# Kernel optimization log

Hardware: AMD Instinct MI355X
Metric: run time of the kernel (lower is better)

## Reference

```python
import jax, jax.numpy as jnp
import numpy as np

TABLE_SIZE = 2 ** 18  # log2_hashmap_size = 18
N_LEVELS = 8
PRIME_Y = np.uint32(2654435761)
PRIME_Z = np.uint32(805459861)
# 8 cube-corner offsets in {0,1}^3
CORNERS = jnp.asarray([[(c >> d) & 1 for d in range(3)] for c in range(8)], dtype=jnp.int32)  # [8,3]


def setup_inputs() -> dict:
    key = jax.random.key(0)
    ks = jax.random.split(key, 6)
    N = 2_097_152
    x = jax.random.uniform(ks[0], (N, 3), dtype=jnp.float32)          # points in [0,1]^3
    mesh_min = jnp.zeros((3,), jnp.float32)
    mesh_max = jnp.ones((3,), jnp.float32)
    # tcnn initializes grid features uniform in [-1e-4, 1e-4]
    tables = jax.random.uniform(ks[1], (N_LEVELS, TABLE_SIZE, 2), jnp.float32, -1e-4, 1e-4)
    w_in = jax.random.normal(ks[2], (16, 64), jnp.float32) * (1.0 / np.sqrt(16))
    w_hidden = jax.random.normal(ks[3], (3, 64, 64), jnp.float32) * (1.0 / np.sqrt(64))
    w_out = jax.random.normal(ks[4], (64, 1), jnp.float32) * (1.0 / np.sqrt(64))
    return {"x": x, "mesh_min": mesh_min, "mesh_max": mesh_max,
            "tables": tables, "w_in": w_in, "w_hidden": w_hidden, "w_out": w_out}


def _hashgrid_encode(u, tables):
    """u: [N,3] in [0,1]. tables: [L, T, F]. Returns [N, L*F]."""
    feats = []
    for l in range(N_LEVELS):
        res = 2 * (2 ** l)  # base_resolution=2, per_level_scale=2
        pos = u * res                                   # [N,3]
        c0 = jnp.floor(pos).astype(jnp.int32)
        w = pos - c0                                    # trilinear fractions, [N,3]
        corners = jnp.clip(c0[:, None, :] + CORNERS[None], 0, res)  # [N,8,3]
        if (res + 1) ** 3 <= TABLE_SIZE:
            # dense grid: no hashing needed at coarse levels
            idx = (corners[..., 0]
                   + corners[..., 1] * (res + 1)
                   + corners[..., 2] * (res + 1) ** 2)
        else:
            uc = corners.astype(jnp.uint32)
            h = uc[..., 0] ^ (uc[..., 1] * PRIME_Y) ^ (uc[..., 2] * PRIME_Z)
            idx = (h % jnp.uint32(TABLE_SIZE)).astype(jnp.int32)
        # trilinear weights per corner: prod over dims of w or (1-w)
        wt = jnp.prod(jnp.where(CORNERS[None] == 1, w[:, None, :], 1.0 - w[:, None, :]), axis=-1)  # [N,8]
        feats.append(jnp.einsum('nc,ncf->nf', wt, tables[l][idx]))  # [N,F]
    return jnp.concatenate(feats, axis=-1)  # [N, L*F] = [N,16]


def reference(x, mesh_min, mesh_max, tables, w_in, w_hidden, w_out):
    u = (x - mesh_min) / (mesh_max - mesh_min)          # normalize to [0,1]^3
    enc = _hashgrid_encode(u, tables)                   # [N,16]
    h = jax.nn.relu(enc @ w_in)                         # [N,64]
    for i in range(w_hidden.shape[0]):                  # 3 more hidden layers (4 total)
        h = jax.nn.relu(h @ w_hidden[i])
    out = (h @ w_out).squeeze(-1)                       # [N], no output activation
    return out
```

## Files before the change

kernel.cpp:

```cpp
#include <hip/hip_runtime.h>
#include <stdint.h>

typedef _Float16 half2v __attribute__((ext_vector_type(2)));
typedef _Float16 half4 __attribute__((ext_vector_type(4)));
typedef _Float16 half8 __attribute__((ext_vector_type(8)));
typedef float floatx4 __attribute__((ext_vector_type(4)));
typedef float float4u __attribute__((ext_vector_type(4), aligned(8)));

#define TPB 256
#define ENC_ROW 20

__device__ __forceinline__ half2v pkrtz(float a, float b) {
    return __builtin_bit_cast(half2v, __builtin_amdgcn_cvt_pkrtz(a, b));
}

__device__ __forceinline__ half4 relu_pack(floatx4 c) {
    half2v lo = pkrtz(fmaxf(c[0], 0.f), fmaxf(c[1], 0.f));
    half2v hi = pkrtz(fmaxf(c[2], 0.f), fmaxf(c[3], 0.f));
    half4 r;
    r[0] = lo[0]; r[1] = lo[1]; r[2] = hi[0]; r[3] = hi[1];
    return r;
}

__global__ void prep_weights(const float* __restrict__ w_in,
                             const float* __restrict__ w_hidden,
                             _Float16* __restrict__ ws) {
    int i = blockIdx.x * 256 + threadIdx.x;
    if (i < 1024) {
        int j = i & 3, lane = (i >> 2) & 63, mt = i >> 8;
        int k = ((lane >> 4) & 3) * 4 + j;
        int n = mt * 16 + (lane & 15);
        ws[i] = (_Float16)w_in[k * 64 + n];
    } else if (i < 13312) {
        int t = i - 1024;
        int j = t & 3, lane = (t >> 2) & 63;
        int mt = (t >> 8) & 3, kt = (t >> 10) & 3, layer = t >> 12;
        int k = kt * 16 + ((lane >> 4) & 3) * 4 + j;
        int n = mt * 16 + (lane & 15);
        ws[i] = (_Float16)w_hidden[layer * 4096 + k * 64 + n];
    }
}

__global__ void prep_tables(const float* __restrict__ tables,
                            uint32_t* __restrict__ tf) {
    int i = blockIdx.x * 256 + threadIdx.x;
    float2 v = ((const float2*)tables)[i];
    half2v h;
    h[0] = (_Float16)(v.x * 8192.f);
    h[1] = (_Float16)(v.y * 8192.f);
    tf[i] = __builtin_bit_cast(uint32_t, h);
}

__global__ __launch_bounds__(TPB, 4) void fused_kernel(
    const float* __restrict__ x,
    const float* __restrict__ mesh_min,
    const float* __restrict__ mesh_max,
    const float* __restrict__ tables,
    const uint32_t* __restrict__ tabs,
    const _Float16* __restrict__ ws,
    const float* __restrict__ w_out,
    float* __restrict__ out,
    int N) {
    __shared__ float2 ltab[881];
    __shared__ uint32_t l3tab[4913];
    __shared__ _Float16 encbuf[4][64][ENC_ROW];

    const int wave = threadIdx.x >> 6;
    const int lane = threadIdx.x & 63;
    const int l15 = lane & 15;
    const int quad = lane >> 4;
    const int wavebase = blockIdx.x * TPB + wave * 64;
    const int p = wavebase + lane;

    {
        const float2* t0 = (const float2*)tables;
        for (int i = threadIdx.x; i < 27; i += TPB) ltab[i] = t0[i];
        const float2* t1 = (const float2*)(tables + 1 * 524288);
        for (int i = threadIdx.x; i < 125; i += TPB) ltab[27 + i] = t1[i];
        const float2* t2 = (const float2*)(tables + 2 * 524288);
        for (int i = threadIdx.x; i < 729; i += TPB) ltab[152 + i] = t2[i];
        const uint32_t* t3 = tabs + 3 * 262144;
        for (int i = threadIdx.x; i < 4913; i += TPB) l3tab[i] = t3[i];
    }

    float mn0 = mesh_min[0], mn1 = mesh_min[1], mn2 = mesh_min[2];
    float mx0 = mesh_max[0], mx1 = mesh_max[1], mx2 = mesh_max[2];
    float ux = (x[3 * p + 0] - mn0) / (mx0 - mn0);
    float uy = (x[3 * p + 1] - mn1) / (mx1 - mn1);
    float uz = (x[3 * p + 2] - mn2) / (mx2 - mn2);

    float ef[16];
    float wl[3][3];
    uint32_t g[24];
    uint32_t g4[8];
    float w4x, w4y, w4z;

#pragma unroll
    for (int l = 0; l < 3; ++l) {
        const int res = 64 << l;
        const uint32_t* tab = tabs + (size_t)(l + 5) * 262144;
        float px = ux * (float)res, py = uy * (float)res, pz = uz * (float)res;
        int cx = (int)floorf(px), cy = (int)floorf(py), cz = (int)floorf(pz);
        wl[l][0] = px - (float)cx;
        wl[l][1] = py - (float)cy;
        wl[l][2] = pz - (float)cz;
        uint32_t hy0 = (uint32_t)cy * 2654435761u, hy1 = (uint32_t)(cy + 1) * 2654435761u;
        uint32_t hz0 = (uint32_t)cz * 805459861u,  hz1 = (uint32_t)(cz + 1) * 805459861u;
#pragma unroll
        for (int c = 0; c < 4; ++c) {
            uint32_t hyz = ((c & 1) ? hy1 : hy0) ^ ((c & 2) ? hz1 : hz0);
            uint32_t i0 = ((uint32_t)cx ^ hyz) & 262143u;
            uint32_t i1 = ((uint32_t)(cx + 1) ^ hyz) & 262143u;
            g[l * 8 + 2 * c + 0] = tab[i0];
            g[l * 8 + 2 * c + 1] = tab[i1];
        }
    }

    {
        const int res = 32, s = 33;
        const uint32_t* tab = tabs + (size_t)4 * 262144;
        float px = ux * 32.f, py = uy * 32.f, pz = uz * 32.f;
        int cx = (int)floorf(px), cy = (int)floorf(py), cz = (int)floorf(pz);
        w4x = px - (float)cx; w4y = py - (float)cy; w4z = pz - (float)cz;
        (void)res;
#pragma unroll
        for (int c = 0; c < 4; ++c) {
            int Y = cy + ((c & 1) ? 1 : 0);
            int Z = cz + ((c & 2) ? 1 : 0);
            int i0 = cx + Y * s + Z * s * s;
            g4[2 * c + 0] = tab[i0];
            g4[2 * c + 1] = tab[i0 + 1];
        }
    }

    __syncthreads();

#pragma unroll
    for (int l = 0; l < 3; ++l) {
        const int res = 2 << l;
        const int s = res + 1;
        const int base = (l == 0) ? 0 : (l == 1) ? 27 : 152;
        float px = ux * (float)res, py = uy * (float)res, pz = uz * (float)res;
        int cx = (int)floorf(px), cy = (int)floorf(py), cz = (int)floorf(pz);
        float wx = px - (float)cx, wy = py - (float)cy, wz = pz - (float)cz;
        float f0 = 0.f, f1 = 0.f;
#pragma unroll
        for (int c = 0; c < 4; ++c) {
            int i0 = base + cx + (cy + ((c & 1) ? 1 : 0)) * s + (cz + ((c & 2) ? 1 : 0)) * s * s;
            float wyz = ((c & 1) ? wy : 1.f - wy) * ((c & 2) ? wz : 1.f - wz);
            float2 e0 = ltab[i0];
            float2 e1 = ltab[i0 + 1];
            f0 += wyz * (e0.x + wx * (e1.x - e0.x));
            f1 += wyz * (e0.y + wx * (e1.y - e0.y));
        }
        ef[2 * l + 0] = f0 * 8192.f;
        ef[2 * l + 1] = f1 * 8192.f;
    }

    {
        const int s = 17;
        float px = ux * 16.f, py = uy * 16.f, pz = uz * 16.f;
        int cx = (int)floorf(px), cy = (int)floorf(py), cz = (int)floorf(pz);
        float wx = px - (float)cx, wy = py - (float)cy, wz = pz - (float)cz;
        float f0 = 0.f, f1 = 0.f;
#pragma unroll
        for (int c = 0; c < 4; ++c) {
            int i0 = cx + (cy + ((c & 1) ? 1 : 0)) * s + (cz + ((c & 2) ? 1 : 0)) * s * s;
            float wyz = ((c & 1) ? wy : 1.f - wy) * ((c & 2) ? wz : 1.f - wz);
            half2v e0 = __builtin_bit_cast(half2v, l3tab[i0]);
            half2v e1 = __builtin_bit_cast(half2v, l3tab[i0 + 1]);
            f0 += wyz * ((float)e0[0] + wx * ((float)e1[0] - (float)e0[0]));
            f1 += wyz * ((float)e0[1] + wx * ((float)e1[1] - (float)e0[1]));
        }
        ef[6] = f0;
        ef[7] = f1;
    }

    {
        float f0 = 0.f, f1 = 0.f;
#pragma unroll
        for (int c = 0; c < 4; ++c) {
            float wyz = ((c & 1) ? w4y : 1.f - w4y) * ((c & 2) ? w4z : 1.f - w4z);
            half2v e0 = __builtin_bit_cast(half2v, g4[2 * c + 0]);
            half2v e1 = __builtin_bit_cast(half2v, g4[2 * c + 1]);
            f0 += wyz * ((float)e0[0] + w4x * ((float)e1[0] - (float)e0[0]));
            f1 += wyz * ((float)e0[1] + w4x * ((float)e1[1] - (float)e0[1]));
        }
        ef[8] = f0;
        ef[9] = f1;
    }

#pragma unroll
    for (int l = 0; l < 3; ++l) {
        float wx = wl[l][0], wy = wl[l][1], wz = wl[l][2];
        float f0 = 0.f, f1 = 0.f;
#pragma unroll
        for (int c = 0; c < 4; ++c) {
            float wyz = ((c & 1) ? wy : 1.f - wy) * ((c & 2) ? wz : 1.f - wz);
            half2v e0 = __builtin_bit_cast(half2v, g[l * 8 + 2 * c + 0]);
            half2v e1 = __builtin_bit_cast(half2v, g[l * 8 + 2 * c + 1]);
            f0 += wyz * ((float)e0[0] + wx * ((float)e1[0] - (float)e0[0]));
            f1 += wyz * ((float)e0[1] + wx * ((float)e1[1] - (float)e0[1]));
        }
        ef[10 + 2 * l + 0] = f0;
        ef[10 + 2 * l + 1] = f1;
    }

#pragma unroll
    for (int v = 0; v < 4; ++v) {
        half2v lo = pkrtz(ef[4 * v + 0], ef[4 * v + 1]);
        half2v hi = pkrtz(ef[4 * v + 2], ef[4 * v + 3]);
        half4 t;
        t[0] = lo[0]; t[1] = lo[1]; t[2] = hi[0]; t[3] = hi[1];
        *(half4*)&encbuf[wave][lane][v * 4] = t;
    }

    floatx4 C[4][4];
    {
        half4 b[4];
#pragma unroll
        for (int nt = 0; nt < 4; ++nt)
            b[nt] = *(const half4*)&encbuf[wave][nt * 16 + l15][quad * 4];
#pragma unroll
        for (int mt = 0; mt < 4; ++mt) {
            half4 a = *(const half4*)(ws + mt * 256 + lane * 4);
#pragma unroll
            for (int nt = 0; nt < 4; ++nt) {
                floatx4 zero = {0.f, 0.f, 0.f, 0.f};
                C[mt][nt] = __builtin_amdgcn_mfma_f32_16x16x16f16(a, b[nt], zero, 0, 0, 0);
            }
        }
    }

#pragma unroll
    for (int layer = 0; layer < 3; ++layer) {
        half4 b[4][4];
#pragma unroll
        for (int kt = 0; kt < 4; ++kt)
#pragma unroll
            for (int nt = 0; nt < 4; ++nt)
                b[kt][nt] = relu_pack(C[kt][nt]);
#pragma unroll
        for (int mt = 0; mt < 4; ++mt) {
            half4 a[4];
#pragma unroll
            for (int kt = 0; kt < 4; ++kt)
                a[kt] = *(const half4*)(ws + 1024 + ((layer * 4 + kt) * 4 + mt) * 256 + lane * 4);
#pragma unroll
            for (int nt = 0; nt < 4; ++nt) {
                floatx4 acc = {0.f, 0.f, 0.f, 0.f};
#pragma unroll
                for (int kt = 0; kt < 4; ++kt)
                    acc = __builtin_amdgcn_mfma_f32_16x16x16f16(a[kt], b[kt][nt], acc, 0, 0, 0);
                C[mt][nt] = acc;
            }
        }
    }

    {
        float s[4] = {0.f, 0.f, 0.f, 0.f};
#pragma unroll
        for (int mt = 0; mt < 4; ++mt) {
            float4 wo = *(const float4*)(w_out + mt * 16 + quad * 4);
#pragma unroll
            for (int nt = 0; nt < 4; ++nt) {
                s[nt] = fmaf(fmaxf(C[mt][nt][0], 0.f), wo.x, s[nt]);
                s[nt] = fmaf(fmaxf(C[mt][nt][1], 0.f), wo.y, s[nt]);
                s[nt] = fmaf(fmaxf(C[mt][nt][2], 0.f), wo.z, s[nt]);
                s[nt] = fmaf(fmaxf(C[mt][nt][3], 0.f), wo.w, s[nt]);
            }
        }
#pragma unroll
        for (int nt = 0; nt < 4; ++nt) {
            s[nt] += __shfl_xor(s[nt], 16, 64);
            s[nt] += __shfl_xor(s[nt], 32, 64);
        }
        float r = (quad & 1) ? ((quad & 2) ? s[3] : s[1])
                             : ((quad & 2) ? s[2] : s[0]);
        out[wavebase + quad * 16 + l15] = r * (1.f / 8192.f);
    }
}

__global__ __launch_bounds__(TPB, 4) void hashgrid_mlp_kernel(
    const float* __restrict__ x,
    const float* __restrict__ mesh_min,
    const float* __restrict__ mesh_max,
    const float* __restrict__ tables,
    const _Float16* __restrict__ ws,
    const float* __restrict__ w_out,
    float* __restrict__ out,
    int N) {
    __shared__ float2 ltab[881];
    __shared__ _Float16 encbuf[4][64][ENC_ROW];

    const int wave = threadIdx.x >> 6;
    const int lane = threadIdx.x & 63;
    const int l15 = lane & 15;
    const int quad = lane >> 4;
    const int wavebase = blockIdx.x * TPB + wave * 64;
    const int p = wavebase + lane;

    {
        const float2* t0 = (const float2*)tables;
        for (int i = threadIdx.x; i < 27; i += TPB) ltab[i] = t0[i];
        const float2* t1 = (const float2*)(tables + 1 * 524288);
        for (int i = threadIdx.x; i < 125; i += TPB) ltab[27 + i] = t1[i];
        const float2* t2 = (const float2*)(tables + 2 * 524288);
        for (int i = threadIdx.x; i < 729; i += TPB) ltab[152 + i] = t2[i];
    }

    float mn0 = mesh_min[0], mn1 = mesh_min[1], mn2 = mesh_min[2];
    float mx0 = mesh_max[0], mx1 = mesh_max[1], mx2 = mesh_max[2];
    float ux = (x[3 * p + 0] - mn0) / (mx0 - mn0);
    float uy = (x[3 * p + 1] - mn1) / (mx1 - mn1);
    float uz = (x[3 * p + 2] - mn2) / (mx2 - mn2);

    float ef[16];
    float wl[3][3];
    float2 g[24];

#pragma unroll
    for (int l = 0; l < 3; ++l) {
        const int res = 64 << l;
        const float* tab = tables + (size_t)(l + 5) * 524288;
        float px = ux * (float)res, py = uy * (float)res, pz = uz * (float)res;
        int cx = (int)floorf(px), cy = (int)floorf(py), cz = (int)floorf(pz);
        wl[l][0] = px - (float)cx;
        wl[l][1] = py - (float)cy;
        wl[l][2] = pz - (float)cz;
        uint32_t hy0 = (uint32_t)cy * 2654435761u, hy1 = (uint32_t)(cy + 1) * 2654435761u;
        uint32_t hz0 = (uint32_t)cz * 805459861u,  hz1 = (uint32_t)(cz + 1) * 805459861u;
#pragma unroll
        for (int c = 0; c < 4; ++c) {
            uint32_t hyz = ((c & 1) ? hy1 : hy0) ^ ((c & 2) ? hz1 : hz0);
            uint32_t i0 = ((uint32_t)cx ^ hyz) & 262143u;
            uint32_t i1 = ((uint32_t)(cx + 1) ^ hyz) & 262143u;
            g[l * 8 + 2 * c + 0] = *(const float2*)(tab + 2 * (size_t)i0);
            g[l * 8 + 2 * c + 1] = *(const float2*)(tab + 2 * (size_t)i1);
        }
    }

#pragma unroll
    for (int l = 3; l < 5; ++l) {
        const int res = 2 << l;
        const int s = res + 1;
        const float* tab = tables + (size_t)l * 524288;
        float px = ux * (float)res, py = uy * (float)res, pz = uz * (float)res;
        int cx = (int)floorf(px), cy = (int)floorf(py), cz = (int)floorf(pz);
        float wx = px - (float)cx, wy = py - (float)cy, wz = pz - (float)cz;
        float f0 = 0.f, f1 = 0.f;
#pragma unroll
        for (int c = 0; c < 4; ++c) {
            int Y = cy + ((c & 1) ? 1 : 0);
            int Z = cz + ((c & 2) ? 1 : 0);
            float wyz = ((c & 1) ? wy : 1.f - wy) * ((c & 2) ? wz : 1.f - wz);
            int i0 = cx + Y * s + Z * s * s;
            float4u v = *(const float4u*)(tab + 2 * (size_t)i0);
            f0 += wyz * (v.x + wx * (v.z - v.x));
            f1 += wyz * (v.y + wx * (v.w - v.y));
        }
        ef[2 * l + 0] = f0;
        ef[2 * l + 1] = f1;
    }

    __syncthreads();

#pragma unroll
    for (int l = 0; l < 3; ++l) {
        const int res = 2 << l;
        const int s = res + 1;
        const int base = (l == 0) ? 0 : (l == 1) ? 27 : 152;
        float px = ux * (float)res, py = uy * (float)res, pz = uz * (float)res;
        int cx = (int)floorf(px), cy = (int)floorf(py), cz = (int)floorf(pz);
        float wx = px - (float)cx, wy = py - (float)cy, wz = pz - (float)cz;
        float f0 = 0.f, f1 = 0.f;
#pragma unroll
        for (int c = 0; c < 4; ++c) {
            int i0 = base + cx + (cy + ((c & 1) ? 1 : 0)) * s + (cz + ((c & 2) ? 1 : 0)) * s * s;
            float wyz = ((c & 1) ? wy : 1.f - wy) * ((c & 2) ? wz : 1.f - wz);
            float2 e0 = ltab[i0];
            float2 e1 = ltab[i0 + 1];
            f0 += wyz * (e0.x + wx * (e1.x - e0.x));
            f1 += wyz * (e0.y + wx * (e1.y - e0.y));
        }
        ef[2 * l + 0] = f0;
        ef[2 * l + 1] = f1;
    }

#pragma unroll
    for (int l = 0; l < 3; ++l) {
        float wx = wl[l][0], wy = wl[l][1], wz = wl[l][2];
        float f0 = 0.f, f1 = 0.f;
#pragma unroll
        for (int c = 0; c < 4; ++c) {
            float wyz = ((c & 1) ? wy : 1.f - wy) * ((c & 2) ? wz : 1.f - wz);
            float2 e0 = g[l * 8 + 2 * c + 0];
            float2 e1 = g[l * 8 + 2 * c + 1];
            f0 += wyz * (e0.x + wx * (e1.x - e0.x));
            f1 += wyz * (e0.y + wx * (e1.y - e0.y));
        }
        ef[10 + 2 * l + 0] = f0;
        ef[10 + 2 * l + 1] = f1;
    }

#pragma unroll
    for (int v = 0; v < 4; ++v) {
        half2v lo = pkrtz(ef[4 * v + 0] * 8192.f, ef[4 * v + 1] * 8192.f);
        half2v hi = pkrtz(ef[4 * v + 2] * 8192.f, ef[4 * v + 3] * 8192.f);
        half4 t;
        t[0] = lo[0]; t[1] = lo[1]; t[2] = hi[0]; t[3] = hi[1];
        *(half4*)&encbuf[wave][lane][v * 4] = t;
    }

    floatx4 C[4][4];
    {
        half4 b[4];
#pragma unroll
        for (int nt = 0; nt < 4; ++nt)
            b[nt] = *(const half4*)&encbuf[wave][nt * 16 + l15][quad * 4];
#pragma unroll
        for (int mt = 0; mt < 4; ++mt) {
            half4 a = *(const half4*)(ws + mt * 256 + lane * 4);
#pragma unroll
            for (int nt = 0; nt < 4; ++nt) {
                floatx4 zero = {0.f, 0.f, 0.f, 0.f};
                C[mt][nt] = __builtin_amdgcn_mfma_f32_16x16x16f16(a, b[nt], zero, 0, 0, 0);
            }
        }
    }

#pragma unroll
    for (int layer = 0; layer < 3; ++layer) {
        half4 b[4][4];
#pragma unroll
        for (int kt = 0; kt < 4; ++kt)
#pragma unroll
            for (int nt = 0; nt < 4; ++nt)
                b[kt][nt] = relu_pack(C[kt][nt]);
#pragma unroll
        for (int mt = 0; mt < 4; ++mt) {
            half4 a[4];
#pragma unroll
            for (int kt = 0; kt < 4; ++kt)
                a[kt] = *(const half4*)(ws + 1024 + ((layer * 4 + kt) * 4 + mt) * 256 + lane * 4);
#pragma unroll
            for (int nt = 0; nt < 4; ++nt) {
                floatx4 acc = {0.f, 0.f, 0.f, 0.f};
#pragma unroll
                for (int kt = 0; kt < 4; ++kt)
                    acc = __builtin_amdgcn_mfma_f32_16x16x16f16(a[kt], b[kt][nt], acc, 0, 0, 0);
                C[mt][nt] = acc;
            }
        }
    }

    {
        float s[4] = {0.f, 0.f, 0.f, 0.f};
#pragma unroll
        for (int mt = 0; mt < 4; ++mt) {
            float4 wo = *(const float4*)(w_out + mt * 16 + quad * 4);
#pragma unroll
            for (int nt = 0; nt < 4; ++nt) {
                s[nt] = fmaf(fmaxf(C[mt][nt][0], 0.f), wo.x, s[nt]);
                s[nt] = fmaf(fmaxf(C[mt][nt][1], 0.f), wo.y, s[nt]);
                s[nt] = fmaf(fmaxf(C[mt][nt][2], 0.f), wo.z, s[nt]);
                s[nt] = fmaf(fmaxf(C[mt][nt][3], 0.f), wo.w, s[nt]);
            }
        }
#pragma unroll
        for (int nt = 0; nt < 4; ++nt) {
            s[nt] += __shfl_xor(s[nt], 16, 64);
            s[nt] += __shfl_xor(s[nt], 32, 64);
        }
        float r = (quad & 1) ? ((quad & 2) ? s[3] : s[1])
                             : ((quad & 2) ? s[2] : s[0]);
        out[wavebase + quad * 16 + l15] = r * (1.f / 8192.f);
    }
}

extern "C" void kernel_launch(void* const* d_in, const int* in_sizes, int n_in,
                              void* d_out, int out_size, void* d_ws,
                              size_t ws_size, hipStream_t stream) {
    const float* x        = (const float*)d_in[0];
    const float* mesh_min = (const float*)d_in[1];
    const float* mesh_max = (const float*)d_in[2];
    const float* tables   = (const float*)d_in[3];
    const float* w_in     = (const float*)d_in[4];
    const float* w_hidden = (const float*)d_in[5];
    const float* w_out    = (const float*)d_in[6];
    float* out = (float*)d_out;
    _Float16* ws = (_Float16*)d_ws;

    int N = out_size;

    hipLaunchKernelGGL(prep_weights, dim3(52), dim3(256), 0, stream,
                       w_in, w_hidden, ws);

    size_t need = 32768 + (size_t)8 * 262144 * 4;
    if (ws_size >= need) {
        uint32_t* tf = (uint32_t*)((char*)d_ws + 32768);
        hipLaunchKernelGGL(prep_tables, dim3(8192), dim3(256), 0, stream,
                           tables, tf);
        hipLaunchKernelGGL(fused_kernel, dim3(N / TPB), dim3(TPB), 0, stream,
                           x, mesh_min, mesh_max, tables, tf, ws, w_out, out, N);
    } else {
        hipLaunchKernelGGL(hashgrid_mlp_kernel, dim3(N / TPB), dim3(TPB), 0, stream,
                           x, mesh_min, mesh_max, tables, ws, w_out, out, N);
    }
}
```

Baseline: 269.8 us.

## Alias encode buffer over lookup tables in LDS, raise occupancy, merge prep kernels

The shared-memory encode buffer now overlays the coarse-level lookup tables in a single union-style LDS block, with a barrier added before the overlay is written. LDS per block shrinks from roughly 36KB to about 26.7KB, and the launch bound rises from 4 to 6 blocks per CU so more waves can hide gather latency. The table-conversion and weight-prep kernels are merged into one launch to remove a kernel launch. The risks are an extra __syncthreads and register spills under the tighter register budget.

Result: slower. 524.3 us (+94.3%).

```diff
diff --git a/kernel.cpp b/kernel.cpp
--- a/kernel.cpp
+++ b/kernel.cpp
@@ -20,6 +20,37 @@
     half4 r;
     r[0] = lo[0]; r[1] = lo[1]; r[2] = hi[0]; r[3] = hi[1];
     return r;
+}
+
+__global__ void prep_all(const float* __restrict__ tables,
+                         uint32_t* __restrict__ tf,
+                         const float* __restrict__ w_in,
+                         const float* __restrict__ w_hidden,
+                         _Float16* __restrict__ ws) {
+    int b = blockIdx.x;
+    if (b < 8192) {
+        int i = b * 256 + threadIdx.x;
+        float2 v = ((const float2*)tables)[i];
+        half2v h;
+        h[0] = (_Float16)(v.x * 8192.f);
+        h[1] = (_Float16)(v.y * 8192.f);
+        tf[i] = __builtin_bit_cast(uint32_t, h);
+    } else {
+        int i = (b - 8192) * 256 + threadIdx.x;
+        if (i < 1024) {
+            int j = i & 3, lane = (i >> 2) & 63, mt = i >> 8;
+            int k = ((lane >> 4) & 3) * 4 + j;
+            int n = mt * 16 + (lane & 15);
+            ws[i] = (_Float16)w_in[k * 64 + n];
+        } else if (i < 13312) {
+            int t = i - 1024;
+            int j = t & 3, lane = (t >> 2) & 63;
+            int mt = (t >> 8) & 3, kt = (t >> 10) & 3, layer = t >> 12;
+            int k = kt * 16 + ((lane >> 4) & 3) * 4 + j;
+            int n = mt * 16 + (lane & 15);
+            ws[i] = (_Float16)w_hidden[layer * 4096 + k * 64 + n];
+        }
+    }
 }
 
 __global__ void prep_weights(const float* __restrict__ w_in,
@@ -41,17 +72,7 @@
     }
 }
 
-__global__ void prep_tables(const float* __restrict__ tables,
-                            uint32_t* __restrict__ tf) {
-    int i = blockIdx.x * 256 + threadIdx.x;
-    float2 v = ((const float2*)tables)[i];
-    half2v h;
-    h[0] = (_Float16)(v.x * 8192.f);
-    h[1] = (_Float16)(v.y * 8192.f);
-    tf[i] = __builtin_bit_cast(uint32_t, h);
-}
-
-__global__ __launch_bounds__(TPB, 4) void fused_kernel(
+__global__ __launch_bounds__(TPB, 6) void fused_kernel(
     const float* __restrict__ x,
     const float* __restrict__ mesh_min,
     const float* __restrict__ mesh_max,
@@ -61,9 +82,10 @@
     const float* __restrict__ w_out,
     float* __restrict__ out,
     int N) {
-    __shared__ float2 ltab[881];
-    __shared__ uint32_t l3tab[4913];
-    __shared__ _Float16 encbuf[4][64][ENC_ROW];
+    __shared__ __align__(16) char smem[26700];
+    float2* ltab = (float2*)smem;
+    uint32_t* l3tab = (uint32_t*)(smem + 7048);
+    _Float16 (*encbuf)[64][ENC_ROW] = (_Float16 (*)[64][ENC_ROW])smem;
 
     const int wave = threadIdx.x >> 6;
     const int lane = threadIdx.x & 63;
@@ -117,12 +139,11 @@
     }
 
     {
-        const int res = 32, s = 33;
+        const int s = 33;
         const uint32_t* tab = tabs + (size_t)4 * 262144;
         float px = ux * 32.f, py = uy * 32.f, pz = uz * 32.f;
         int cx = (int)floorf(px), cy = (int)floorf(py), cz = (int)floorf(pz);
         w4x = px - (float)cx; w4y = py - (float)cy; w4z = pz - (float)cz;
-        (void)res;
 #pragma unroll
         for (int c = 0; c < 4; ++c) {
             int Y = cy + ((c & 1) ? 1 : 0);
@@ -205,6 +226,8 @@
         ef[10 + 2 * l + 0] = f0;
         ef[10 + 2 * l + 1] = f1;
     }
+
+    __syncthreads();
 
 #pragma unroll
     for (int v = 0; v < 4; ++v) {
@@ -493,17 +516,16 @@
 
     int N = out_size;
 
-    hipLaunchKernelGGL(prep_weights, dim3(52), dim3(256), 0, stream,
-                       w_in, w_hidden, ws);
-
     size_t need = 32768 + (size_t)8 * 262144 * 4;
     if (ws_size >= need) {
         uint32_t* tf = (uint32_t*)((char*)d_ws + 32768);
-        hipLaunchKernelGGL(prep_tables, dim3(8192), dim3(256), 0, stream,
-                           tables, tf);
+        hipLaunchKernelGGL(prep_all, dim3(8244), dim3(256), 0, stream,
+                           tables, tf, w_in, w_hidden, ws);
         hipLaunchKernelGGL(fused_kernel, dim3(N / TPB), dim3(TPB), 0, stream,
                            x, mesh_min, mesh_max, tables, tf, ws, w_out, out, N);
     } else {
+        hipLaunchKernelGGL(prep_weights, dim3(52), dim3(256), 0, stream,
+                           w_in, w_hidden, ws);
         hipLaunchKernelGGL(hashgrid_mlp_kernel, dim3(N / TPB), dim3(TPB), 0, stream,
                            x, mesh_min, mesh_max, tables, ws, w_out, out, N);
     }
```
